# Performance work log

Hardware: AMD Instinct MI355X
Metric: run time of the kernel (lower is better)

The kernel has to match this reference:

```python
import jax, jax.numpy as jnp
import numpy as np

NUM_HEADS = 8
OUT_DIM = 64
HEAD_DIM = OUT_DIM // NUM_HEADS
ALPHA = 0.2  # leaky_relu negative slope


def setup_inputs() -> dict:
    key = jax.random.key(0)
    k1, k2, k3, k4 = jax.random.split(key, 4)
    N, E, IN_DIM = 20000, 4000, 128
    X = jax.random.normal(k1, (N, IN_DIM), dtype=jnp.float32)
    H = jax.random.randint(k2, (N, E), 0, 2, dtype=jnp.int32)  # binary incidence
    # Linear weight (stored [in, out]; equivalent to torch x @ W.T)
    W = jax.random.normal(k3, (IN_DIM, OUT_DIM), dtype=jnp.float32) * (1.0 / np.sqrt(IN_DIM))
    attention = jax.random.normal(k4, (1, NUM_HEADS, 2 * HEAD_DIM), dtype=jnp.float32) * 0.1
    bias = jnp.zeros((OUT_DIM,), dtype=jnp.float32)
    return {"X": X, "H": H, "W": W, "attention": attention, "bias": bias}


def reference(X, H, W, attention, bias):
    N, E = H.shape
    mask = (H > 0).astype(X.dtype)                       # [N, E] membership
    Xh = (X @ W).reshape(N, NUM_HEADS, HEAD_DIM)          # [N, h, d]
    # Original keeps only the self pairwise score: att . concat(x_i, x_i)
    a = attention[0, :, :HEAD_DIM] + attention[0, :, HEAD_DIM:]  # [h, d]
    s = jax.nn.leaky_relu(jnp.einsum('nhd,hd->nh', Xh, a), ALPHA)  # [N, h]
    # Per-hyperedge softmax over member nodes (stable via global per-head max)
    expn = jnp.exp(s - jnp.max(s, axis=0, keepdims=True))          # [N, h]
    denom = jnp.einsum('ne,nh->eh', mask, expn)                    # [E, h]
    weighted = expn[:, :, None] * Xh                               # [N, h, d]
    num = jnp.einsum('ne,nhd->ehd', mask, weighted)                # [E, h, d]
    safe = jnp.where(denom > 0, denom, 1.0)
    agg = jnp.where((denom > 0)[:, :, None], num / safe[:, :, None], 0.0)  # [E, h, d]
    # Scatter the edge aggregate back to every member node
    out = jnp.einsum('ne,ehd->nhd', mask, agg).reshape(N, OUT_DIM) + bias
    return out
```

## Files before the change

kernel.cpp:

```cpp
#include <hip/hip_runtime.h>
#include <math.h>

#define N_NODES 20000
#define N_EDGES 4000
#define IN_DIM 128
#define NUM_HEADS 8
#define ALPHA 0.2f

#define HB_W 64
#define HBT_W 320
#define KPAD1 20480
#define KPAD2 4096
#define IPAD1 4096
#define IPAD2 20224
#define SPLITS1 32
#define SPLITS2 8

typedef float f32x4 __attribute__((ext_vector_type(4)));
typedef __bf16 bf16x8 __attribute__((ext_vector_type(8)));


__device__ __forceinline__ unsigned short f2b(float f) {
    unsigned u = __float_as_uint(f);
    return (unsigned short)((u + 0x7FFFu + ((u >> 16) & 1u)) >> 16);
}

__global__ void __launch_bounds__(256) kA(const int* __restrict__ H,
                                          unsigned long long* __restrict__ Hb,
                                          const float* __restrict__ X,
                                          const float* __restrict__ W,
                                          const float* __restrict__ att,
                                          float* __restrict__ expn,
                                          float* __restrict__ Yv) {
    int role = blockIdx.x & 1;
    int bid = blockIdx.x >> 1;
    if (role == 0) {
        int wq = threadIdx.x >> 6;
        int lane = threadIdx.x & 63;
        int n = bid * 4 + wq;
        const int* hrow = H + (size_t)n * N_EDGES;
        unsigned long long* brow = Hb + (size_t)n * HB_W;
        int g = lane >> 4;
        int sh = 4 * (lane & 15);
        for (int it = 0; it < 16; it += 2) {
            int e0 = it * 256 + lane * 4;
            int e1 = e0 + 256;
            unsigned long long v0 = 0ull, v1 = 0ull;
            if (e0 < N_EDGES) {
                int4 v = *(const int4*)(hrow + e0);
                unsigned nb = (v.x > 0 ? 1u : 0u) | (v.y > 0 ? 2u : 0u) |
                              (v.z > 0 ? 4u : 0u) | (v.w > 0 ? 8u : 0u);
                v0 = (unsigned long long)nb << sh;
            }
            if (e1 < N_EDGES) {
                int4 v = *(const int4*)(hrow + e1);
                unsigned nb = (v.x > 0 ? 1u : 0u) | (v.y > 0 ? 2u : 0u) |
                              (v.z > 0 ? 4u : 0u) | (v.w > 0 ? 8u : 0u);
                v1 = (unsigned long long)nb << sh;
            }
            v0 |= __shfl_xor(v0, 1, 64);  v1 |= __shfl_xor(v1, 1, 64);
            v0 |= __shfl_xor(v0, 2, 64);  v1 |= __shfl_xor(v1, 2, 64);
            v0 |= __shfl_xor(v0, 4, 64);  v1 |= __shfl_xor(v1, 4, 64);
            v0 |= __shfl_xor(v0, 8, 64);  v1 |= __shfl_xor(v1, 8, 64);
            if ((lane & 15) == 0) {
                brow[it * 4 + g] = v0;
                brow[it * 4 + 4 + g] = v1;
            }
        }
    } else {
        int t = bid * 256 + threadIdx.x;
        int n = __builtin_amdgcn_readfirstlane(t >> 6);
        int d = t & 63;
        const float* x = X + (size_t)n * IN_DIM;
        float acc = 0.f;
#pragma unroll 8
        for (int k = 0; k < IN_DIM; k++) acc += x[k] * W[k * 64 + d];
        int h = d >> 3, j = d & 7;
        float av = att[h * 16 + j] + att[h * 16 + 8 + j];
        float v = acc * av;
        v += __shfl_xor(v, 1, 64);
        v += __shfl_xor(v, 2, 64);
        v += __shfl_xor(v, 4, 64);
        float s = (v >= 0.f) ? v : ALPHA * v;
        float e = expf(s);
        Yv[(size_t)n * 64 + d] = e * acc;
        if (j == 0) expn[(size_t)n * NUM_HEADS + h] = e;
    }
}

__global__ void __launch_bounds__(256) kB(const unsigned long long* __restrict__ Hb,
                                          unsigned long long* __restrict__ HbT,
                                          const float* __restrict__ Yv,
                                          const float* __restrict__ expn,
                                          unsigned short* __restrict__ VtT1) {
    __shared__ float tl[64][65];
    if (blockIdx.x < 320) {
        int t = threadIdx.x;
        int n0 = blockIdx.x * 64;
        int r = t >> 2, s4 = t & 3;
#pragma unroll
        for (int m = 0; m < 4; m++) {
            int cbase = s4 * 16 + m * 4;
            float4 v = make_float4(0.f, 0.f, 0.f, 0.f);
            if (n0 + r < N_NODES) v = *(const float4*)(Yv + (size_t)(n0 + r) * 64 + cbase);
            tl[r][cbase] = v.x; tl[r][cbase + 1] = v.y; tl[r][cbase + 2] = v.z; tl[r][cbase + 3] = v.w;
        }
        __syncthreads();
        int d = t >> 2;
        unsigned short buf[16];
#pragma unroll
        for (int j = 0; j < 16; j++) buf[j] = f2b(tl[s4 * 16 + j][d]);
        uint4* o = (uint4*)(VtT1 + (size_t)d * KPAD1 + n0 + s4 * 16);
        o[0] = *(uint4*)&buf[0];
        o[1] = *(uint4*)&buf[8];
        int nl = t & 63;
        int rw = t >> 6;
#pragma unroll
        for (int p = 0; p < 4; p++) {
            int row = 64 + rw * 4 + p;
            float v = 0.f;
            if (row < 72 && n0 + nl < N_NODES) v = expn[(size_t)(n0 + nl) * NUM_HEADS + (row - 64)];
            VtT1[(size_t)row * KPAD1 + n0 + nl] = f2b(v);
        }
    } else {
        int b = blockIdx.x - 320;
        int bx = b % 313;
        int by = b / 313;
        int wq = threadIdx.x >> 6;
        int lane = threadIdx.x & 63;
        int et = by * 4 + wq;
        if (et >= 63) return;
        int n0 = bx * 64;
        int n = n0 + lane;
        unsigned long long w = (n < N_NODES) ? Hb[(size_t)n * HB_W + et] : 0ull;
        unsigned long long out = 0ull;
#pragma unroll
        for (int c = 0; c < 64; c++) {
            unsigned long long bb = __ballot((w >> c) & 1ull);
            if (lane == c) out = bb;
        }
        int e = et * 64 + lane;
        if (e < N_EDGES) HbT[(size_t)e * HBT_W + bx] = out;
    }
}

__device__ __forceinline__ bf16x8 expand8(unsigned b) {
    union { uint4 u; bf16x8 v; } cv;
    cv.u.x = ((b & 1u)   ? 0x3F80u : 0u) | ((b & 2u)   ? 0x3F800000u : 0u);
    cv.u.y = ((b & 4u)   ? 0x3F80u : 0u) | ((b & 8u)   ? 0x3F800000u : 0u);
    cv.u.z = ((b & 16u)  ? 0x3F80u : 0u) | ((b & 32u)  ? 0x3F800000u : 0u);
    cv.u.w = ((b & 64u)  ? 0x3F80u : 0u) | ((b & 128u) ? 0x3F800000u : 0u);
    return cv.v;
}
__device__ __forceinline__ bf16x8 ldsread(const unsigned short* p) {
    union { uint4 u; bf16x8 v; } cv;
    cv.u = *(const uint4*)p;
    return cv.v;
}

template <int NCT>
__global__ void __launch_bounds__(256) k_mm(const unsigned long long* __restrict__ bits,
                                            int stride, int I,
                                            const unsigned short* __restrict__ Vg,
                                            int Kpad, int kPerSplit,
                                            float* __restrict__ P, int Ipad) {
    __shared__ __align__(16) unsigned short VldsF[NCT * 4 * 64 * 8];
    const int t = threadIdx.x;
    const int l = t & 63;
    const int w = t >> 6;
    const int q = l >> 4;
    const int cl = l & 15;
    const int rowbase = blockIdx.x * 256 + w * 64;
    const int k0 = blockIdx.y * kPerSplit;
    const int nstages = kPerSplit >> 7;

    const unsigned long long* bp[4];
#pragma unroll
    for (int rt = 0; rt < 4; rt++) {
        int r = rowbase + rt * 16 + cl;
        if (r >= I) r = I - 1;
        bp[rt] = bits + (size_t)r * stride;
    }

    f32x4 acc[4][NCT];
#pragma unroll
    for (int rt = 0; rt < 4; rt++)
#pragma unroll
        for (int c = 0; c < NCT; c++) acc[rt][c] = (f32x4){0.f, 0.f, 0.f, 0.f};

    for (int st = 0; st < nstages; st++) {
        int kc = k0 + st * 128;
        __syncthreads();
#pragma unroll
        for (int c = 0; c < NCT; c++) {
            uint4 val = *(const uint4*)(Vg + (size_t)(c * 16 + cl) * Kpad + kc + (w * 4 + q) * 8);
            *(uint4*)&VldsF[(((c * 4 + w) * 64) + l) * 8] = val;
        }
        ulonglong2 wb[4];
#pragma unroll
        for (int rt = 0; rt < 4; rt++) wb[rt] = *(const ulonglong2*)(bp[rt] + (kc >> 6));
        __syncthreads();
#pragma unroll
        for (int kf = 0; kf < 4; kf++) {
            bf16x8 a[4];
#pragma unroll
            for (int rt = 0; rt < 4; rt++) {
                unsigned long long wsel = (kf < 2) ? wb[rt].x : wb[rt].y;
                unsigned byte = (unsigned)(wsel >> ((kf & 1) * 32 + q * 8)) & 0xFFu;
                a[rt] = expand8(byte);
            }
#pragma unroll
            for (int c = 0; c < NCT; c++) {
                bf16x8 bv = ldsread(&VldsF[(((c * 4 + kf) * 64) + l) * 8]);
#pragma unroll
                for (int rt = 0; rt < 4; rt++)
                    acc[rt][c] = __builtin_amdgcn_mfma_f32_16x16x32_bf16(a[rt], bv, acc[rt][c], 0, 0, 0);
            }
        }
    }

    size_t base = (size_t)blockIdx.y * Ipad;
#pragma unroll
    for (int rt = 0; rt < 4; rt++)
#pragma unroll
        for (int c = 0; c < NCT; c++)
#pragma unroll
            for (int r = 0; r < 4; r++)
                P[(base + rowbase + rt * 16 + q * 4 + r) * (NCT * 16) + c * 16 + cl] = acc[rt][c][r];
}

__global__ void __launch_bounds__(256) k_aggT(const float* __restrict__ P1,
                                              unsigned short* __restrict__ VtT2) {
    __shared__ float tl[64][65];
    int t = threadIdx.x;
    int e0 = blockIdx.x * 64;
    int el = t >> 2, s4 = t & 3;
    int e = e0 + el;
    float num[16];
#pragma unroll
    for (int j = 0; j < 16; j++) num[j] = 0.f;
    float den0 = 0.f, den1 = 0.f;
    for (int sp = 0; sp < SPLITS1; sp++) {
        const float* row = P1 + ((size_t)sp * IPAD1 + e) * 80;
        const float4* r4 = (const float4*)(row + s4 * 16);
        float4 a = r4[0], b = r4[1], c = r4[2], d = r4[3];
        num[0] += a.x;  num[1] += a.y;  num[2] += a.z;  num[3] += a.w;
        num[4] += b.x;  num[5] += b.y;  num[6] += b.z;  num[7] += b.w;
        num[8] += c.x;  num[9] += c.y;  num[10] += c.z; num[11] += c.w;
        num[12] += d.x; num[13] += d.y; num[14] += d.z; num[15] += d.w;
        float2 dn = *(const float2*)(row + 64 + s4 * 2);
        den0 += dn.x; den1 += dn.y;
    }
#pragma unroll
    for (int j = 0; j < 16; j++) {
        float den = (j < 8) ? den0 : den1;
        float v = (e < N_EDGES && den > 0.f) ? num[j] / den : 0.f;
        tl[el][s4 * 16 + j] = v;
    }
    __syncthreads();
    int d = t >> 2;
    unsigned short buf[16];
#pragma unroll
    for (int j = 0; j < 16; j++) buf[j] = f2b(tl[s4 * 16 + j][d]);
    uint4* o = (uint4*)(VtT2 + (size_t)d * KPAD2 + e0 + s4 * 16);
    o[0] = *(uint4*)&buf[0];
    o[1] = *(uint4*)&buf[8];
}

__global__ void __launch_bounds__(256) k_final4(const float* __restrict__ P2,
                                                const float* __restrict__ bias,
                                                float* __restrict__ out) {
    int t = blockIdx.x * blockDim.x + threadIdx.x;
    int n = t >> 4, c4 = t & 15;
    float4 v = *(const float4*)(bias + c4 * 4);
#pragma unroll
    for (int sp = 0; sp < SPLITS2; sp++) {
        float4 p = *(const float4*)(P2 + ((size_t)sp * IPAD2 + n) * 64 + c4 * 4);
        v.x += p.x; v.y += p.y; v.z += p.z; v.w += p.w;
    }
    *(float4*)(out + (size_t)n * 64 + c4 * 4) = v;
}

extern "C" void kernel_launch(void* const* d_in, const int* in_sizes, int n_in,
                              void* d_out, int out_size, void* d_ws, size_t ws_size,
                              hipStream_t stream) {
    const float* X = (const float*)d_in[0];
    const int* H = (const int*)d_in[1];
    const float* W = (const float*)d_in[2];
    const float* att = (const float*)d_in[3];
    const float* bias = (const float*)d_in[4];
    float* out = (float*)d_out;

    char* ws = (char*)d_ws;
    unsigned long long* Hb  = (unsigned long long*)(ws + 0);
    unsigned long long* HbT = (unsigned long long*)(ws + 10240000);
    unsigned short* VtT1 = (unsigned short*)(ws + 20480000);
    unsigned short* VtT2 = (unsigned short*)(ws + 23756800);
    float* expn = (float*)(ws + 24281088);
    float* Yv   = (float*)(ws + 24921088);
    float* P    = (float*)(ws + 30041088);

    kA<<<10000, 256, 0, stream>>>(H, Hb, X, W, att, expn, Yv);
    kB<<<5328, 256, 0, stream>>>(Hb, HbT, Yv, expn, VtT1);
    k_mm<5><<<dim3(IPAD1 / 256, SPLITS1), 256, 0, stream>>>(HbT, HBT_W, N_EDGES, VtT1,
                                                            KPAD1, KPAD1 / SPLITS1, P, IPAD1);
    k_aggT<<<KPAD2 / 64, 256, 0, stream>>>(P, VtT2);
    k_mm<4><<<dim3(IPAD2 / 256, SPLITS2), 256, 0, stream>>>(Hb, HB_W, N_NODES, VtT2,
                                                            KPAD2, KPAD2 / SPLITS2, P, IPAD2);
    k_final4<<<1250, 256, 0, stream>>>(P, bias, out);
}
```

Baseline: 534.0 us.

## Fuse all stages into one cooperative persistent kernel with grid syncs

```diff
diff --git a/kernel.cpp b/kernel.cpp
--- a/kernel.cpp
+++ b/kernel.cpp
@@ -1,5 +1,8 @@
 #include <hip/hip_runtime.h>
+#include <hip/hip_cooperative_groups.h>
 #include <math.h>
+
+namespace cg = cooperative_groups;
 
 #define N_NODES 20000
 #define N_EDGES 4000
@@ -24,126 +27,6 @@
     unsigned u = __float_as_uint(f);
     return (unsigned short)((u + 0x7FFFu + ((u >> 16) & 1u)) >> 16);
 }
-
-__global__ void __launch_bounds__(256) kA(const int* __restrict__ H,
-                                          unsigned long long* __restrict__ Hb,
-                                          const float* __restrict__ X,
-                                          const float* __restrict__ W,
-                                          const float* __restrict__ att,
-                                          float* __restrict__ expn,
-                                          float* __restrict__ Yv) {
-    int role = blockIdx.x & 1;
-    int bid = blockIdx.x >> 1;
-    if (role == 0) {
-        int wq = threadIdx.x >> 6;
-        int lane = threadIdx.x & 63;
-        int n = bid * 4 + wq;
-        const int* hrow = H + (size_t)n * N_EDGES;
-        unsigned long long* brow = Hb + (size_t)n * HB_W;
-        int g = lane >> 4;
-        int sh = 4 * (lane & 15);
-        for (int it = 0; it < 16; it += 2) {
-            int e0 = it * 256 + lane * 4;
-            int e1 = e0 + 256;
-            unsigned long long v0 = 0ull, v1 = 0ull;
-            if (e0 < N_EDGES) {
-                int4 v = *(const int4*)(hrow + e0);
-                unsigned nb = (v.x > 0 ? 1u : 0u) | (v.y > 0 ? 2u : 0u) |
-                              (v.z > 0 ? 4u : 0u) | (v.w > 0 ? 8u : 0u);
-                v0 = (unsigned long long)nb << sh;
-            }
-            if (e1 < N_EDGES) {
-                int4 v = *(const int4*)(hrow + e1);
-                unsigned nb = (v.x > 0 ? 1u : 0u) | (v.y > 0 ? 2u : 0u) |
-                              (v.z > 0 ? 4u : 0u) | (v.w > 0 ? 8u : 0u);
-                v1 = (unsigned long long)nb << sh;
-            }
-            v0 |= __shfl_xor(v0, 1, 64);  v1 |= __shfl_xor(v1, 1, 64);
-            v0 |= __shfl_xor(v0, 2, 64);  v1 |= __shfl_xor(v1, 2, 64);
-            v0 |= __shfl_xor(v0, 4, 64);  v1 |= __shfl_xor(v1, 4, 64);
-            v0 |= __shfl_xor(v0, 8, 64);  v1 |= __shfl_xor(v1, 8, 64);
-            if ((lane & 15) == 0) {
-                brow[it * 4 + g] = v0;
-                brow[it * 4 + 4 + g] = v1;
-            }
-        }
-    } else {
-        int t = bid * 256 + threadIdx.x;
-        int n = __builtin_amdgcn_readfirstlane(t >> 6);
-        int d = t & 63;
-        const float* x = X + (size_t)n * IN_DIM;
-        float acc = 0.f;
-#pragma unroll 8
-        for (int k = 0; k < IN_DIM; k++) acc += x[k] * W[k * 64 + d];
-        int h = d >> 3, j = d & 7;
-        float av = att[h * 16 + j] + att[h * 16 + 8 + j];
-        float v = acc * av;
-        v += __shfl_xor(v, 1, 64);
-        v += __shfl_xor(v, 2, 64);
-        v += __shfl_xor(v, 4, 64);
-        float s = (v >= 0.f) ? v : ALPHA * v;
-        float e = expf(s);
-        Yv[(size_t)n * 64 + d] = e * acc;
-        if (j == 0) expn[(size_t)n * NUM_HEADS + h] = e;
-    }
-}
-
-__global__ void __launch_bounds__(256) kB(const unsigned long long* __restrict__ Hb,
-                                          unsigned long long* __restrict__ HbT,
-                                          const float* __restrict__ Yv,
-                                          const float* __restrict__ expn,
-                                          unsigned short* __restrict__ VtT1) {
-    __shared__ float tl[64][65];
-    if (blockIdx.x < 320) {
-        int t = threadIdx.x;
-        int n0 = blockIdx.x * 64;
-        int r = t >> 2, s4 = t & 3;
-#pragma unroll
-        for (int m = 0; m < 4; m++) {
-            int cbase = s4 * 16 + m * 4;
-            float4 v = make_float4(0.f, 0.f, 0.f, 0.f);
-            if (n0 + r < N_NODES) v = *(const float4*)(Yv + (size_t)(n0 + r) * 64 + cbase);
-            tl[r][cbase] = v.x; tl[r][cbase + 1] = v.y; tl[r][cbase + 2] = v.z; tl[r][cbase + 3] = v.w;
-        }
-        __syncthreads();
-        int d = t >> 2;
-        unsigned short buf[16];
-#pragma unroll
-        for (int j = 0; j < 16; j++) buf[j] = f2b(tl[s4 * 16 + j][d]);
-        uint4* o = (uint4*)(VtT1 + (size_t)d * KPAD1 + n0 + s4 * 16);
-        o[0] = *(uint4*)&buf[0];
-        o[1] = *(uint4*)&buf[8];
-        int nl = t & 63;
-        int rw = t >> 6;
-#pragma unroll
-        for (int p = 0; p < 4; p++) {
-            int row = 64 + rw * 4 + p;
-            float v = 0.f;
-            if (row < 72 && n0 + nl < N_NODES) v = expn[(size_t)(n0 + nl) * NUM_HEADS + (row - 64)];
-            VtT1[(size_t)row * KPAD1 + n0 + nl] = f2b(v);
-        }
-    } else {
-        int b = blockIdx.x - 320;
-        int bx = b % 313;
-        int by = b / 313;
-        int wq = threadIdx.x >> 6;
-        int lane = threadIdx.x & 63;
-        int et = by * 4 + wq;
-        if (et >= 63) return;
-        int n0 = bx * 64;
-        int n = n0 + lane;
-        unsigned long long w = (n < N_NODES) ? Hb[(size_t)n * HB_W + et] : 0ull;
-        unsigned long long out = 0ull;
-#pragma unroll
-        for (int c = 0; c < 64; c++) {
-            unsigned long long bb = __ballot((w >> c) & 1ull);
-            if (lane == c) out = bb;
-        }
-        int e = et * 64 + lane;
-        if (e < N_EDGES) HbT[(size_t)e * HBT_W + bx] = out;
-    }
-}
-
 __device__ __forceinline__ bf16x8 expand8(unsigned b) {
     union { uint4 u; bf16x8 v; } cv;
     cv.u.x = ((b & 1u)   ? 0x3F80u : 0u) | ((b & 2u)   ? 0x3F800000u : 0u);
@@ -158,20 +41,134 @@
     return cv.v;
 }
 
+
+__device__ __forceinline__ void body_pack(int bid, int tid, const int* __restrict__ H,
+                                          unsigned long long* __restrict__ Hb) {
+    int wq = tid >> 6;
+    int lane = tid & 63;
+    int n = bid * 4 + wq;
+    const int* hrow = H + (size_t)n * N_EDGES;
+    unsigned long long* brow = Hb + (size_t)n * HB_W;
+    int g = lane >> 4;
+    int sh = 4 * (lane & 15);
+    for (int it = 0; it < 16; it += 2) {
+        int e0 = it * 256 + lane * 4;
+        int e1 = e0 + 256;
+        unsigned long long v0 = 0ull, v1 = 0ull;
+        if (e0 < N_EDGES) {
+            int4 v = *(const int4*)(hrow + e0);
+            unsigned nb = (v.x > 0 ? 1u : 0u) | (v.y > 0 ? 2u : 0u) |
+                          (v.z > 0 ? 4u : 0u) | (v.w > 0 ? 8u : 0u);
+            v0 = (unsigned long long)nb << sh;
+        }
+        if (e1 < N_EDGES) {
+            int4 v = *(const int4*)(hrow + e1);
+            unsigned nb = (v.x > 0 ? 1u : 0u) | (v.y > 0 ? 2u : 0u) |
+                          (v.z > 0 ? 4u : 0u) | (v.w > 0 ? 8u : 0u);
+            v1 = (unsigned long long)nb << sh;
+        }
+        v0 |= __shfl_xor(v0, 1, 64);  v1 |= __shfl_xor(v1, 1, 64);
+        v0 |= __shfl_xor(v0, 2, 64);  v1 |= __shfl_xor(v1, 2, 64);
+        v0 |= __shfl_xor(v0, 4, 64);  v1 |= __shfl_xor(v1, 4, 64);
+        v0 |= __shfl_xor(v0, 8, 64);  v1 |= __shfl_xor(v1, 8, 64);
+        if ((lane & 15) == 0) {
+            brow[it * 4 + g] = v0;
+            brow[it * 4 + 4 + g] = v1;
+        }
+    }
+}
+
+__device__ __forceinline__ void body_fused1(int bid, int tid, const float* __restrict__ X,
+                                            const float* __restrict__ W,
+                                            const float* __restrict__ att,
+                                            float* __restrict__ expn,
+                                            float* __restrict__ Yv) {
+    int t = bid * 256 + tid;
+    int n = __builtin_amdgcn_readfirstlane(t >> 6);
+    int d = t & 63;
+    const float* x = X + (size_t)n * IN_DIM;
+    float acc = 0.f;
+#pragma unroll 8
+    for (int k = 0; k < IN_DIM; k++) acc += x[k] * W[k * 64 + d];
+    int h = d >> 3, j = d & 7;
+    float av = att[h * 16 + j] + att[h * 16 + 8 + j];
+    float v = acc * av;
+    v += __shfl_xor(v, 1, 64);
+    v += __shfl_xor(v, 2, 64);
+    v += __shfl_xor(v, 4, 64);
+    float s = (v >= 0.f) ? v : ALPHA * v;
+    float e = expf(s);
+    Yv[(size_t)n * 64 + d] = e * acc;
+    if (j == 0) expn[(size_t)n * NUM_HEADS + h] = e;
+}
+
+__device__ __forceinline__ void body_transFE(int bid, int tid, float* tl ,
+                                             const float* __restrict__ Yv,
+                                             const float* __restrict__ expn,
+                                             unsigned short* __restrict__ VtT1) {
+    int n0 = bid * 64;
+    int r = tid >> 2, s4 = tid & 3;
+#pragma unroll
+    for (int m = 0; m < 4; m++) {
+        int cbase = s4 * 16 + m * 4;
+        float4 v = make_float4(0.f, 0.f, 0.f, 0.f);
+        if (n0 + r < N_NODES) v = *(const float4*)(Yv + (size_t)(n0 + r) * 64 + cbase);
+        tl[r * 65 + cbase] = v.x; tl[r * 65 + cbase + 1] = v.y;
+        tl[r * 65 + cbase + 2] = v.z; tl[r * 65 + cbase + 3] = v.w;
+    }
+    __syncthreads();
+    int d = tid >> 2;
+    unsigned short buf[16];
+#pragma unroll
+    for (int j = 0; j < 16; j++) buf[j] = f2b(tl[(s4 * 16 + j) * 65 + d]);
+    uint4* o = (uint4*)(VtT1 + (size_t)d * KPAD1 + n0 + s4 * 16);
+    o[0] = *(uint4*)&buf[0];
+    o[1] = *(uint4*)&buf[8];
+    int nl = tid & 63;
+    int rw = tid >> 6;
+#pragma unroll
+    for (int p = 0; p < 4; p++) {
+        int row = 64 + rw * 4 + p;
+        float v = 0.f;
+        if (row < 72 && n0 + nl < N_NODES) v = expn[(size_t)(n0 + nl) * NUM_HEADS + (row - 64)];
+        VtT1[(size_t)row * KPAD1 + n0 + nl] = f2b(v);
+    }
+}
+
+__device__ __forceinline__ void body_transB(int bx, int by, int tid,
+                                            const unsigned long long* __restrict__ Hb,
+                                            unsigned long long* __restrict__ HbT) {
+    int wq = tid >> 6;
+    int lane = tid & 63;
+    int et = by * 4 + wq;
+    if (et < 63) {
+        int n0 = bx * 64;
+        int n = n0 + lane;
+        unsigned long long w = (n < N_NODES) ? Hb[(size_t)n * HB_W + et] : 0ull;
+        unsigned long long out = 0ull;
+#pragma unroll
+        for (int c = 0; c < 64; c++) {
+            unsigned long long bb = __ballot((w >> c) & 1ull);
+            if (lane == c) out = bb;
+        }
+        int e = et * 64 + lane;
+        if (e < N_EDGES) HbT[(size_t)e * HBT_W + bx] = out;
+    }
+}
+
 template <int NCT>
-__global__ void __launch_bounds__(256) k_mm(const unsigned long long* __restrict__ bits,
-                                            int stride, int I,
-                                            const unsigned short* __restrict__ Vg,
-                                            int Kpad, int kPerSplit,
-                                            float* __restrict__ P, int Ipad) {
-    __shared__ __align__(16) unsigned short VldsF[NCT * 4 * 64 * 8];
-    const int t = threadIdx.x;
-    const int l = t & 63;
-    const int w = t >> 6;
+__device__ __forceinline__ void body_mm(int bx, int by, int tid, unsigned short* VldsF,
+                                        const unsigned long long* __restrict__ bits,
+                                        int stride, int I,
+                                        const unsigned short* __restrict__ Vg,
+                                        int Kpad, int kPerSplit,
+                                        float* __restrict__ P, int Ipad) {
+    const int l = tid & 63;
+    const int w = tid >> 6;
     const int q = l >> 4;
     const int cl = l & 15;
-    const int rowbase = blockIdx.x * 256 + w * 64;
-    const int k0 = blockIdx.y * kPerSplit;
+    const int rowbase = bx * 256 + w * 64;
+    const int k0 = by * kPerSplit;
     const int nstages = kPerSplit >> 7;
 
     const unsigned long long* bp[4];
@@ -219,7 +216,7 @@
         }
     }
 
-    size_t base = (size_t)blockIdx.y * Ipad;
+    size_t base = (size_t)by * Ipad;
 #pragma unroll
     for (int rt = 0; rt < 4; rt++)
 #pragma unroll
@@ -229,12 +226,11 @@
                 P[(base + rowbase + rt * 16 + q * 4 + r) * (NCT * 16) + c * 16 + cl] = acc[rt][c][r];
 }
 
-__global__ void __launch_bounds__(256) k_aggT(const float* __restrict__ P1,
-                                              unsigned short* __restrict__ VtT2) {
-    __shared__ float tl[64][65];
-    int t = threadIdx.x;
-    int e0 = blockIdx.x * 64;
-    int el = t >> 2, s4 = t & 3;
+__device__ __forceinline__ void body_aggT(int bid, int tid, float* tl ,
+                                          const float* __restrict__ P1,
+                                          unsigned short* __restrict__ VtT2) {
+    int e0 = bid * 64;
+    int el = tid >> 2, s4 = tid & 3;
     int e = e0 + el;
     float num[16];
 #pragma unroll
@@ -255,37 +251,122 @@
     for (int j = 0; j < 16; j++) {
         float den = (j < 8) ? den0 : den1;
         float v = (e < N_EDGES && den > 0.f) ? num[j] / den : 0.f;
-        tl[el][s4 * 16 + j] = v;
+        tl[el * 65 + s4 * 16 + j] = v;
     }
     __syncthreads();
-    int d = t >> 2;
+    int d = tid >> 2;
     unsigned short buf[16];
 #pragma unroll
-    for (int j = 0; j < 16; j++) buf[j] = f2b(tl[s4 * 16 + j][d]);
+    for (int j = 0; j < 16; j++) buf[j] = f2b(tl[(s4 * 16 + j) * 65 + d]);
     uint4* o = (uint4*)(VtT2 + (size_t)d * KPAD2 + e0 + s4 * 16);
     o[0] = *(uint4*)&buf[0];
     o[1] = *(uint4*)&buf[8];
 }
 
+__device__ __forceinline__ void body_final4(int bid, int tid, const float* __restrict__ P2,
+                                            const float* __restrict__ bias,
+                                            float* __restrict__ out) {
+    int t = bid * 256 + tid;
+    int n = t >> 4, c4 = t & 15;
+    float4 v = *(const float4*)(bias + c4 * 4);
+#pragma unroll
+    for (int sp = 0; sp < SPLITS2; sp++) {
+        float4 p = *(const float4*)(P2 + ((size_t)sp * IPAD2 + n) * 64 + c4 * 4);
+        v.x += p.x; v.y += p.y; v.z += p.z; v.w += p.w;
+    }
+    *(float4*)(out + (size_t)n * 64 + c4 * 4) = v;
+}
+
+__global__ void __launch_bounds__(256) mega(const int* __restrict__ H,
+                                            unsigned long long* __restrict__ Hb,
+                                            unsigned long long* __restrict__ HbT,
+                                            const float* __restrict__ X,
+                                            const float* __restrict__ W,
+                                            const float* __restrict__ att,
+                                            const float* __restrict__ bias,
+                                            unsigned short* __restrict__ VtT1,
+                                            unsigned short* __restrict__ VtT2,
+                                            float* __restrict__ expn,
+                                            float* __restrict__ Yv,
+                                            float* __restrict__ P,
+                                            float* __restrict__ out) {
+    __shared__ __align__(16) char smem[20480];
+    cg::grid_group grid = cg::this_grid();
+    const int tid = threadIdx.x;
+    const int G = gridDim.x;
+
+    for (int v = blockIdx.x; v < 10000; v += G) {
+        if ((v & 1) == 0) body_pack(v >> 1, tid, H, Hb);
+        else              body_fused1(v >> 1, tid, X, W, att, expn, Yv);
+    }
+    grid.sync();
+    for (int v = blockIdx.x; v < 5328; v += G) {
+        if (v < 320) body_transFE(v, tid, (float*)smem, Yv, expn, VtT1);
+        else { int b = v - 320; body_transB(b % 313, b / 313, tid, Hb, HbT); }
+        __syncthreads();
+    }
+    grid.sync();
+    for (int v = blockIdx.x; v < 16 * SPLITS1; v += G)
+        body_mm<5>(v % 16, v / 16, tid, (unsigned short*)smem, HbT, HBT_W, N_EDGES,
+                   VtT1, KPAD1, KPAD1 / SPLITS1, P, IPAD1);
+    grid.sync();
+    for (int v = blockIdx.x; v < 64; v += G) {
+        body_aggT(v, tid, (float*)smem, P, VtT2);
+        __syncthreads();
+    }
+    grid.sync();
+    for (int v = blockIdx.x; v < 79 * SPLITS2; v += G)
+        body_mm<4>(v % 79, v / 79, tid, (unsigned short*)smem, Hb, HB_W, N_NODES,
+                   VtT2, KPAD2, KPAD2 / SPLITS2, P, IPAD2);
+    grid.sync();
+    for (int v = blockIdx.x; v < 1250; v += G)
+        body_final4(v, tid, P, bias, out);
+}
+
+__global__ void __launch_bounds__(256) kA(const int* __restrict__ H,
+                                          unsigned long long* __restrict__ Hb,
+                                          const float* __restrict__ X,
+                                          const float* __restrict__ W,
+                                          const float* __restrict__ att,
+                                          float* __restrict__ expn,
+                                          float* __restrict__ Yv) {
+    if ((blockIdx.x & 1) == 0) body_pack(blockIdx.x >> 1, threadIdx.x, H, Hb);
+    else body_fused1(blockIdx.x >> 1, threadIdx.x, X, W, att, expn, Yv);
+}
+__global__ void __launch_bounds__(256) kB(const unsigned long long* __restrict__ Hb,
+                                          unsigned long long* __restrict__ HbT,
+                                          const float* __restrict__ Yv,
+                                          const float* __restrict__ expn,
+                                          unsigned short* __restrict__ VtT1) {
+    __shared__ float tl[64 * 65];
+    if (blockIdx.x < 320) body_transFE(blockIdx.x, threadIdx.x, tl, Yv, expn, VtT1);
+    else { int b = blockIdx.x - 320; body_transB(b % 313, b / 313, threadIdx.x, Hb, HbT); }
+}
+template <int NCT>
+__global__ void __launch_bounds__(256) k_mm(const unsigned long long* __restrict__ bits,
+                                            int stride, int I,
+                                            const unsigned short* __restrict__ Vg,
+                                            int Kpad, int kPerSplit,
+                                            float* __restrict__ P, int Ipad) {
+    __shared__ __align__(16) unsigned short VldsF[NCT * 4 * 64 * 8];
+    body_mm<NCT>(blockIdx.x, blockIdx.y, threadIdx.x, VldsF, bits, stride, I, Vg, Kpad, kPerSplit, P, Ipad);
+}
+__global__ void __launch_bounds__(256) k_aggT(const float* __restrict__ P1,
+                                              unsigned short* __restrict__ VtT2) {
+    __shared__ float tl[64 * 65];
+    body_aggT(blockIdx.x, threadIdx.x, tl, P1, VtT2);
+}
 __global__ void __launch_bounds__(256) k_final4(const float* __restrict__ P2,
                                                 const float* __restrict__ bias,
                                                 float* __restrict__ out) {
-    int t = blockIdx.x * blockDim.x + threadIdx.x;
-    int n = t >> 4, c4 = t & 15;
-    float4 v = *(const float4*)(bias + c4 * 4);
-#pragma unroll
-    for (int sp = 0; sp < SPLITS2; sp++) {
-        float4 p = *(const float4*)(P2 + ((size_t)sp * IPAD2 + n) * 64 + c4 * 4);
-        v.x += p.x; v.y += p.y; v.z += p.z; v.w += p.w;
-    }
-    *(float4*)(out + (size_t)n * 64 + c4 * 4) = v;
+    body_final4(blockIdx.x, threadIdx.x, P2, bias, out);
 }
 
 extern "C" void kernel_launch(void* const* d_in, const int* in_sizes, int n_in,
                               void* d_out, int out_size, void* d_ws, size_t ws_size,
                               hipStream_t stream) {
+    const int* H = (const int*)d_in[1];
     const float* X = (const float*)d_in[0];
-    const int* H = (const int*)d_in[1];
     const float* W = (const float*)d_in[2];
     const float* att = (const float*)d_in[3];
     const float* bias = (const float*)d_in[4];
@@ -300,12 +381,26 @@
     float* Yv   = (float*)(ws + 24921088);
     float* P    = (float*)(ws + 30041088);
 
-    kA<<<10000, 256, 0, stream>>>(H, Hb, X, W, att, expn, Yv);
-    kB<<<5328, 256, 0, stream>>>(Hb, HbT, Yv, expn, VtT1);
-    k_mm<5><<<dim3(IPAD1 / 256, SPLITS1), 256, 0, stream>>>(HbT, HBT_W, N_EDGES, VtT1,
-                                                            KPAD1, KPAD1 / SPLITS1, P, IPAD1);
-    k_aggT<<<KPAD2 / 64, 256, 0, stream>>>(P, VtT2);
-    k_mm<4><<<dim3(IPAD2 / 256, SPLITS2), 256, 0, stream>>>(Hb, HB_W, N_NODES, VtT2,
-                                                            KPAD2, KPAD2 / SPLITS2, P, IPAD2);
-    k_final4<<<1250, 256, 0, stream>>>(P, bias, out);
-}
+    hipError_t err = hipErrorUnknown;
+    int maxB = 0;
+    if (hipOccupancyMaxActiveBlocksPerMultiprocessor(&maxB, (const void*)mega, 256, 0) == hipSuccess
+        && maxB > 0) {
+        int grid = maxB * 256;
+        if (grid > 2048) grid = 2048;
+        void* args[] = {(void*)&H, (void*)&Hb, (void*)&HbT, (void*)&X, (void*)&W,
+                        (void*)&att, (void*)&bias, (void*)&VtT1, (void*)&VtT2,
+                        (void*)&expn, (void*)&Yv, (void*)&P, (void*)&out};
+        err = hipLaunchCooperativeKernel((const void*)mega, dim3(grid), dim3(256),
+                                         args, 0, stream);
+    }
+    if (err != hipSuccess) {
+        kA<<<10000, 256, 0, stream>>>(H, Hb, X, W, att, expn, Yv);
+        kB<<<5328, 256, 0, stream>>>(Hb, HbT, Yv, expn, VtT1);
+        k_mm<5><<<dim3(16, SPLITS1), 256, 0, stream>>>(HbT, HBT_W, N_EDGES, VtT1,
+                                                       KPAD1, KPAD1 / SPLITS1, P, IPAD1);
+        k_aggT<<<64, 256, 0, stream>>>(P, VtT2);
+        k_mm<4><<<dim3(79, SPLITS2), 256, 0, stream>>>(Hb, HB_W, N_NODES, VtT2,
+                                                       KPAD2, KPAD2 / SPLITS2, P, IPAD2);
+        k_final4<<<1250, 256, 0, stream>>>(P, bias, out);
+    }
+}
```

Measured after the change: 535.0 us. Within noise of the previous version (+0.2%).
